# Kernel optimization log

Measured on AMD Instinct MI355X. Metric: run time of the kernel, lower is better.

Reference implementation:

```python
import jax, jax.numpy as jnp
import numpy as np

NEG_INF = -1e9  # Keras uses a large negative for masked logits


def setup_inputs() -> dict:
    key = jax.random.key(0)
    k1, k2, k3, k4, k5 = jax.random.split(key, 5)
    B, Tq, Tv, D, U = 8, 128, 128, 512, 1024
    query = jax.random.normal(k1, (B, Tq, D), dtype=jnp.float32)
    value = jax.random.normal(k2, (B, Tv, D), dtype=jnp.float32)
    mask = jnp.ones((B, Tv), dtype=bool)
    # Dense(units, use_bias=False) kernels and AdditiveAttention scale vector
    W1 = jax.random.normal(k3, (D, U), dtype=jnp.float32) * (1.0 / np.sqrt(D))
    W2 = jax.random.normal(k4, (D, U), dtype=jnp.float32) * (1.0 / np.sqrt(D))
    scale = jax.random.normal(k5, (U,), dtype=jnp.float32) * (1.0 / np.sqrt(U))
    return {"query": query, "value": value, "mask": mask,
            "W1": W1, "W2": W2, "scale": scale}


def reference(query, value, mask, W1, W2, scale):
    # Projections (Dense, no bias)
    wq = jnp.einsum('btd,du->btu', query, W1)   # [B, Tq, U]
    wk = jnp.einsum('bsd,du->bsu', value, W2)   # [B, Tv, U]
    # Additive (Bahdanau) scores: sum_u scale_u * tanh(wq + wk)
    # Materializes [B, Tq, Tv, U] broadcast-add like Keras AdditiveAttention.
    scores = jnp.einsum('u,btsu->bts', scale,
                        jnp.tanh(wq[:, :, None, :] + wk[:, None, :, :]))
    # value mask over key axis (query_mask is all-ones in the source -> no-op)
    scores = jnp.where(mask[:, None, :], scores, NEG_INF)
    attn = jax.nn.softmax(scores, axis=-1)       # [B, Tq, Tv]
    context = jnp.einsum('bts,bsd->btd', attn, value)  # [B, Tq, D]
    return context, attn
```

## Files before the change

kernel.cpp:

```cpp
#include <hip/hip_runtime.h>

#define B_  8
#define TQ  128
#define TV  128
#define DIM 512
#define UU  1024
#define NSPLIT 16
#define NP  (B_ * TQ * TV)
#define C2  2.885390081777927f

typedef __attribute__((ext_vector_type(8))) short     short8;
typedef __attribute__((ext_vector_type(4))) float     f32x4;
typedef __attribute__((ext_vector_type(4))) unsigned short us4;

__device__ __forceinline__ unsigned short bf16_rtne(float x) {
    unsigned u = __float_as_uint(x);
    unsigned r = u + 0x7FFF + ((u >> 16) & 1);
    return (unsigned short)(r >> 16);
}

__global__ __launch_bounds__(256) void k_prep(
    const float* __restrict__ Q, const float* __restrict__ Vv,
    const float* __restrict__ W1, const float* __restrict__ W2,
    unsigned short* __restrict__ Ab, unsigned short* __restrict__ Wh)
{
    __shared__ float ts[32][36];
    const int bx = blockIdx.x;
    const int t  = threadIdx.x;

    if (bx < 1024) {
        int idx = bx * 256 + t;
        int mat = idx >> 17;
        const float* src = mat ? Vv : Q;
        int off = (idx & 131071) * 4;
        float4 v = *(const float4*)&src[off];
        us4 h;
        h.x = bf16_rtne(v.x);
        h.y = bf16_rtne(v.y);
        h.z = bf16_rtne(v.z);
        h.w = bf16_rtne(v.w);
        *(us4*)&Ab[mat * 524288 + off] = h;
    } else {
        int b2   = bx - 1024;
        int mat  = b2 >> 9;
        int tile = b2 & 511;
        int n0 = (tile & 31) * 32;
        int k0 = (tile >> 5) * 32;
        const float* W = mat ? W2 : W1;

        int kk = t >> 3, n4 = (t & 7) * 4;
        float4 w = *(const float4*)&W[(k0 + kk) * UU + n0 + n4];
        ts[n4 + 0][kk] = w.x; ts[n4 + 1][kk] = w.y;
        ts[n4 + 2][kk] = w.z; ts[n4 + 3][kk] = w.w;
        __syncthreads();

        int nn = t >> 3, k4 = (t & 7) * 4;
        float4 v = *(const float4*)&ts[nn][k4];
        us4 h;
        h.x = bf16_rtne(v.x);
        h.y = bf16_rtne(v.y);
        h.z = bf16_rtne(v.z);
        h.w = bf16_rtne(v.w);
        unsigned off = mat * 524288 + (n0 + nn) * 512 + k0 + k4;
        *(us4*)&Wh[off] = h;
    }
}

#define PKP 72
__global__ __launch_bounds__(256) void k_proj(
    const unsigned short* __restrict__ Ab, const unsigned short* __restrict__ Bh,
    float* __restrict__ Eq, float* __restrict__ Ek)
{
    __shared__ short sAb[64 * PKP], sBh[64 * PKP];

    const int tid  = threadIdx.x;
    const int wave = tid >> 6;
    const int lane = tid & 63;

    const int flat = blockIdx.x;
    const int x    = flat & 7;
    const int j    = flat >> 3;
    const int pair = x * 4 + (j >> 4);
    const int nt   = pair & 15;
    const int mat  = pair >> 4;
    const int mt   = j & 15;
    const int m0   = mt * 64;
    const int n0   = nt * 64;

    const unsigned mb = mat * 524288u;
    const int wm = (wave & 1) * 32;
    const int wn = (wave >> 1) * 32;

    const int sm = tid >> 2, sg = tid & 3;
    const unsigned short* gA = Ab + mb + (m0 + sm) * 512;
    const unsigned short* gB = Bh + mb + (n0 + sm) * 512;
    const int so0 = sm * PKP + sg * 8;
    const int so1 = sm * PKP + 32 + sg * 8;

    const int fr = lane & 15, fq = lane >> 4;
    const int aOff0 = (wm + fr) * PKP + fq * 8;
    const int aOff1 = (wm + 16 + fr) * PKP + fq * 8;
    const int bOff0 = (wn + fr) * PKP + fq * 8;
    const int bOff1 = (wn + 16 + fr) * PKP + fq * 8;

    f32x4 acc00 = {0.f, 0.f, 0.f, 0.f};
    f32x4 acc01 = {0.f, 0.f, 0.f, 0.f};
    f32x4 acc10 = {0.f, 0.f, 0.f, 0.f};
    f32x4 acc11 = {0.f, 0.f, 0.f, 0.f};

    int4 rA0, rA1, rB0, rB1;
    #define LOADALL(K)                                                       \
        rA0 = *(const int4*)(gA + (K) + sg * 8);                             \
        rA1 = *(const int4*)(gA + (K) + 32 + sg * 8);                        \
        rB0 = *(const int4*)(gB + (K) + sg * 8);                             \
        rB1 = *(const int4*)(gB + (K) + 32 + sg * 8);

    LOADALL(0)

    #pragma unroll 1
    for (int kc = 0; kc < 8; ++kc) {
        *(int4*)&sAb[so0] = rA0;  *(int4*)&sAb[so1] = rA1;
        *(int4*)&sBh[so0] = rB0;  *(int4*)&sBh[so1] = rB1;
        __syncthreads();

        if (kc < 7) { LOADALL((kc + 1) * 64) }

        #pragma unroll
        for (int ks = 0; ks < 2; ++ks) {
            const int o = ks * 32;
            short8 a0 = *(const short8*)&sAb[aOff0 + o];
            short8 a1 = *(const short8*)&sAb[aOff1 + o];
            short8 b0 = *(const short8*)&sBh[bOff0 + o];
            short8 b1 = *(const short8*)&sBh[bOff1 + o];

            acc00 = __builtin_amdgcn_mfma_f32_16x16x32_bf16(a0, b0, acc00, 0, 0, 0);
            acc01 = __builtin_amdgcn_mfma_f32_16x16x32_bf16(a0, b1, acc01, 0, 0, 0);
            acc10 = __builtin_amdgcn_mfma_f32_16x16x32_bf16(a1, b0, acc10, 0, 0, 0);
            acc11 = __builtin_amdgcn_mfma_f32_16x16x32_bf16(a1, b1, acc11, 0, 0, 0);
        }
        __syncthreads();
    }
    #undef LOADALL

    float* C = mat ? Ek : Eq;
    #pragma unroll
    for (int r = 0; r < 4; ++r) {
        int row0 = m0 + wm + fq * 4 + r;
        int row1 = row0 + 16;
        int col0 = n0 + wn + fr;
        C[row0 * UU + col0]      = __builtin_amdgcn_exp2f(C2 * acc00[r]);
        C[row0 * UU + col0 + 16] = __builtin_amdgcn_exp2f(C2 * acc01[r]);
        C[row1 * UU + col0]      = __builtin_amdgcn_exp2f(C2 * acc10[r]);
        C[row1 * UU + col0 + 16] = __builtin_amdgcn_exp2f(C2 * acc11[r]);
    }
}
#undef PKP

__global__ __launch_bounds__(512, 4) void k_scores(
    const float* __restrict__ Eq, const float* __restrict__ Ek,
    const float* __restrict__ scale, float* __restrict__ part)
{
    __shared__ float qs[64][68];
    __shared__ float ks[64][68];
    __shared__ float ss[64];

    const int tid = threadIdx.x;
    const int tx  = tid & 15;
    const int ty  = tid >> 4;
    const int b   = blockIdx.z & 7;
    const int us  = blockIdx.z >> 3;
    const int t0  = blockIdx.y * 64;
    const int s0  = blockIdx.x * 64;
    const int u0  = us * (UU / NSPLIT);

    {
        const int r  = tid >> 3;
        const int c0 = (tid & 7) * 8;
        const float* srq = &Eq[(b * TQ + t0 + r) * UU + u0 + c0];
        const float* srk = &Ek[(b * TV + s0 + r) * UU + u0 + c0];
        const int rp = (r >> 2) | ((r & 3) << 4);
        *(float4*)&qs[r][c0]      = *(const float4*)(srq);
        *(float4*)&qs[r][c0 + 4]  = *(const float4*)(srq + 4);
        *(float4*)&ks[rp][c0]     = *(const float4*)(srk);
        *(float4*)&ks[rp][c0 + 4] = *(const float4*)(srk + 4);
        if (tid < 16)
            *(float4*)&ss[tid * 4] = *(const float4*)&scale[u0 + tid * 4];
    }
    __syncthreads();

    float acc[2][4] = {};

    #pragma unroll 2
    for (int u4 = 0; u4 < 16; ++u4) {
        float4 q[2], k[4];
        q[0] = *(const float4*)&qs[ty * 2][u4 * 4];
        q[1] = *(const float4*)&qs[ty * 2 + 1][u4 * 4];
        #pragma unroll
        for (int jj = 0; jj < 4; ++jj)
            k[jj] = *(const float4*)&ks[tx + (jj << 4)][u4 * 4];
        float4 sv = *(const float4*)&ss[u4 * 4];

        #pragma unroll
        for (int i = 0; i < 2; ++i) {
            #pragma unroll
            for (int jj = 0; jj < 4; ++jj) {
                float b1 = fmaf(q[i].x, k[jj].x, 1.f);
                float b2 = fmaf(q[i].y, k[jj].y, 1.f);
                float n1 = fmaf(sv.y, b1, sv.x * b2);
                acc[i][jj] = fmaf(n1, __builtin_amdgcn_rcpf(b1 * b2), acc[i][jj]);
                float b3 = fmaf(q[i].z, k[jj].z, 1.f);
                float b4 = fmaf(q[i].w, k[jj].w, 1.f);
                float n2 = fmaf(sv.w, b3, sv.z * b4);
                acc[i][jj] = fmaf(n2, __builtin_amdgcn_rcpf(b3 * b4), acc[i][jj]);
            }
        }
    }

    #pragma unroll
    for (int i = 0; i < 2; ++i) {
        float4 o = {acc[i][0], acc[i][1], acc[i][2], acc[i][3]};
        *(float4*)&part[us * NP + (b * TQ + t0 + ty * 2 + i) * TV + s0 + tx * 4] = o;
    }
}

__global__ __launch_bounds__(512) void k_ctx(
    const float* __restrict__ part, const int* __restrict__ mask,
    const float* __restrict__ Vv,
    float* __restrict__ attn, float* __restrict__ ctx)
{
    __shared__ float at[128][20];

    const int tid = threadIdx.x;
    const int dc  = blockIdx.x;
    const int tt  = blockIdx.y;
    const int b   = blockIdx.z;
    const int t0  = tt * 16;

    const int rg = tid >> 5;
    const int ln = tid & 31;
    const int base = (b * TQ + t0 + rg) * TV;

    float4 p4 = {0.f, 0.f, 0.f, 0.f};
    #pragma unroll
    for (int i = 0; i < NSPLIT; ++i) {
        float4 v = *(const float4*)&part[i * NP + base + ln * 4];
        p4.x += v.x; p4.y += v.y; p4.z += v.z; p4.w += v.w;
    }
    const int4 mk = *(const int4*)&mask[b * TV + ln * 4];
    float x[4];
    x[0] = mk.x ? -2.f * p4.x : -1e9f;
    x[1] = mk.y ? -2.f * p4.y : -1e9f;
    x[2] = mk.z ? -2.f * p4.z : -1e9f;
    x[3] = mk.w ? -2.f * p4.w : -1e9f;

    float m = fmaxf(fmaxf(x[0], x[1]), fmaxf(x[2], x[3]));
    #pragma unroll
    for (int o = 16; o > 0; o >>= 1) m = fmaxf(m, __shfl_xor(m, o, 32));
    const float L2E = 1.4426950408889634f;
    float e[4], sum = 0.f;
    #pragma unroll
    for (int j = 0; j < 4; ++j) {
        e[j] = __builtin_amdgcn_exp2f((x[j] - m) * L2E);
        sum += e[j];
    }
    #pragma unroll
    for (int o = 16; o > 0; o >>= 1) sum += __shfl_xor(sum, o, 32);
    const float r = __builtin_amdgcn_rcpf(sum);

    float4 av = {e[0] * r, e[1] * r, e[2] * r, e[3] * r};
    at[ln * 4 + 0][rg] = av.x;
    at[ln * 4 + 1][rg] = av.y;
    at[ln * 4 + 2][rg] = av.z;
    at[ln * 4 + 3][rg] = av.w;
    if (dc == 0) *(float4*)&attn[base + ln * 4] = av;
    __syncthreads();

    const int d  = (tid & 127) + dc * 128;
    const int tg = tid >> 7;
    float acc[4] = {};
    const float* vp = &Vv[b * TV * DIM + d];
    #pragma unroll 4
    for (int s = 0; s < TV; ++s) {
        float v  = vp[s * DIM];
        float4 a = *(const float4*)&at[s][tg * 4];
        acc[0] = fmaf(a.x, v, acc[0]);
        acc[1] = fmaf(a.y, v, acc[1]);
        acc[2] = fmaf(a.z, v, acc[2]);
        acc[3] = fmaf(a.w, v, acc[3]);
    }
    #pragma unroll
    for (int j = 0; j < 4; ++j) {
        int t = t0 + tg * 4 + j;
        ctx[(b * TQ + t) * DIM + d] = acc[j];
    }
}

extern "C" void kernel_launch(void* const* d_in, const int* in_sizes, int n_in,
                              void* d_out, int out_size, void* d_ws, size_t ws_size,
                              hipStream_t stream)
{
    const float* query = (const float*)d_in[0];
    const float* value = (const float*)d_in[1];
    const int*   mask  = (const int*)d_in[2];
    const float* W1    = (const float*)d_in[3];
    const float* W2    = (const float*)d_in[4];
    const float* scale = (const float*)d_in[5];

    float* out  = (float*)d_out;
    float* ctx  = out;
    float* attn = out + B_ * TQ * DIM;

    float* Eq   = (float*)d_ws;
    float* Ek   = Eq + 1024 * 1024;
    float* part = Ek + 1024 * 1024;
    unsigned short* Ab = (unsigned short*)(part + NSPLIT * NP);
    unsigned short* Wh = Ab + 2 * 1024 * 512;

    hipLaunchKernelGGL(k_prep,   dim3(2048),             dim3(256), 0, stream,
                       query, value, W1, W2, Ab, Wh);
    hipLaunchKernelGGL(k_proj,   dim3(512),              dim3(256), 0, stream,
                       Ab, Wh, Eq, Ek);
    hipLaunchKernelGGL(k_scores, dim3(2, 2, 8 * NSPLIT), dim3(512), 0, stream,
                       Eq, Ek, scale, part);
    hipLaunchKernelGGL(k_ctx,    dim3(4, 8, 8),          dim3(512), 0, stream,
                       part, mask, value, attn, ctx);
}
```

Before: 110.3 us.

## Use packed FP32 FMA in scores kernel with transposed K tile and 4x4 outputs

Rewrites the scores kernel to use packed 2-wide FP32 FMA (v_pk_fma_f32 on CDNA) over pairs of key columns, with K stored transposed in shared memory so adjacent keys are contiguous. Each thread now computes 4x4 outputs instead of 2x4, and the block shrinks from 512 to 256 threads. This aims to cut VALU instruction count and LDS loads per output. The cost is more registers per thread, fewer threads per block, and a transposed scalar LDS store pattern that may cause bank conflicts.

```diff
diff --git a/kernel.cpp b/kernel.cpp
--- a/kernel.cpp
+++ b/kernel.cpp
@@ -11,12 +11,17 @@
 
 typedef __attribute__((ext_vector_type(8))) short     short8;
 typedef __attribute__((ext_vector_type(4))) float     f32x4;
+typedef __attribute__((ext_vector_type(2))) float     f32x2;
 typedef __attribute__((ext_vector_type(4))) unsigned short us4;
 
 __device__ __forceinline__ unsigned short bf16_rtne(float x) {
     unsigned u = __float_as_uint(x);
     unsigned r = u + 0x7FFF + ((u >> 16) & 1);
     return (unsigned short)(r >> 16);
+}
+
+__device__ __forceinline__ f32x2 pkfma(f32x2 a, f32x2 b, f32x2 c) {
+    return __builtin_elementwise_fma(a, b, c);
 }
 
 __global__ __launch_bounds__(256) void k_prep(
@@ -156,12 +161,12 @@
 }
 #undef PKP
 
-__global__ __launch_bounds__(512, 4) void k_scores(
+__global__ __launch_bounds__(256) void k_scores(
     const float* __restrict__ Eq, const float* __restrict__ Ek,
     const float* __restrict__ scale, float* __restrict__ part)
 {
     __shared__ float qs[64][68];
-    __shared__ float ks[64][68];
+    __shared__ float ksT[64][68];
     __shared__ float ss[64];
 
     const int tid = threadIdx.x;
@@ -174,52 +179,70 @@
     const int u0  = us * (UU / NSPLIT);
 
     {
-        const int r  = tid >> 3;
-        const int c0 = (tid & 7) * 8;
+        const int r  = tid >> 2;
+        const int c0 = (tid & 3) * 16;
         const float* srq = &Eq[(b * TQ + t0 + r) * UU + u0 + c0];
         const float* srk = &Ek[(b * TV + s0 + r) * UU + u0 + c0];
-        const int rp = (r >> 2) | ((r & 3) << 4);
-        *(float4*)&qs[r][c0]      = *(const float4*)(srq);
-        *(float4*)&qs[r][c0 + 4]  = *(const float4*)(srq + 4);
-        *(float4*)&ks[rp][c0]     = *(const float4*)(srk);
-        *(float4*)&ks[rp][c0 + 4] = *(const float4*)(srk + 4);
+        #pragma unroll
+        for (int i = 0; i < 4; ++i) {
+            *(float4*)&qs[r][c0 + i * 4] = *(const float4*)(srq + i * 4);
+            float4 kv = *(const float4*)(srk + i * 4);
+            ksT[c0 + i * 4 + 0][r] = kv.x;
+            ksT[c0 + i * 4 + 1][r] = kv.y;
+            ksT[c0 + i * 4 + 2][r] = kv.z;
+            ksT[c0 + i * 4 + 3][r] = kv.w;
+        }
         if (tid < 16)
             *(float4*)&ss[tid * 4] = *(const float4*)&scale[u0 + tid * 4];
     }
     __syncthreads();
 
-    float acc[2][4] = {};
+    f32x2 acc[4][2] = {};
+    const f32x2 one2 = {1.f, 1.f};
 
     #pragma unroll 2
     for (int u4 = 0; u4 < 16; ++u4) {
-        float4 q[2], k[4];
-        q[0] = *(const float4*)&qs[ty * 2][u4 * 4];
-        q[1] = *(const float4*)&qs[ty * 2 + 1][u4 * 4];
+        f32x2 kA[4][2];
         #pragma unroll
-        for (int jj = 0; jj < 4; ++jj)
-            k[jj] = *(const float4*)&ks[tx + (jj << 4)][u4 * 4];
-        float4 sv = *(const float4*)&ss[u4 * 4];
+        for (int uu = 0; uu < 4; ++uu) {
+            float4 kv = *(const float4*)&ksT[u4 * 4 + uu][tx * 4];
+            kA[uu][0] = (f32x2){kv.x, kv.y};
+            kA[uu][1] = (f32x2){kv.z, kv.w};
+        }
+        const float4 sv = *(const float4*)&ss[u4 * 4];
+        const f32x2 sL0 = {sv.x, sv.x}, sH0 = {sv.y, sv.y};
+        const f32x2 sL1 = {sv.z, sv.z}, sH1 = {sv.w, sv.w};
 
         #pragma unroll
-        for (int i = 0; i < 2; ++i) {
+        for (int i = 0; i < 4; ++i) {
+            const float4 qv = *(const float4*)&qs[ty * 4 + i][u4 * 4];
+            const f32x2 qL0 = {qv.x, qv.x}, qH0 = {qv.y, qv.y};
+            const f32x2 qL1 = {qv.z, qv.z}, qH1 = {qv.w, qv.w};
+
             #pragma unroll
-            for (int jj = 0; jj < 4; ++jj) {
-                float b1 = fmaf(q[i].x, k[jj].x, 1.f);
-                float b2 = fmaf(q[i].y, k[jj].y, 1.f);
-                float n1 = fmaf(sv.y, b1, sv.x * b2);
-                acc[i][jj] = fmaf(n1, __builtin_amdgcn_rcpf(b1 * b2), acc[i][jj]);
-                float b3 = fmaf(q[i].z, k[jj].z, 1.f);
-                float b4 = fmaf(q[i].w, k[jj].w, 1.f);
-                float n2 = fmaf(sv.w, b3, sv.z * b4);
-                acc[i][jj] = fmaf(n2, __builtin_amdgcn_rcpf(b3 * b4), acc[i][jj]);
+            for (int jp = 0; jp < 2; ++jp) {
+                f32x2 b1 = pkfma(qL0, kA[0][jp], one2);
+                f32x2 b2 = pkfma(qH0, kA[1][jp], one2);
+                f32x2 p  = b1 * b2;
+                f32x2 n  = pkfma(sH0, b1, sL0 * b2);
+                f32x2 r  = {__builtin_amdgcn_rcpf(p.x),
+                            __builtin_amdgcn_rcpf(p.y)};
+                acc[i][jp] = pkfma(n, r, acc[i][jp]);
+                f32x2 b3 = pkfma(qL1, kA[2][jp], one2);
+                f32x2 b4 = pkfma(qH1, kA[3][jp], one2);
+                f32x2 p2 = b3 * b4;
+                f32x2 n2 = pkfma(sH1, b3, sL1 * b4);
+                f32x2 r2 = {__builtin_amdgcn_rcpf(p2.x),
+                            __builtin_amdgcn_rcpf(p2.y)};
+                acc[i][jp] = pkfma(n2, r2, acc[i][jp]);
             }
         }
     }
 
     #pragma unroll
-    for (int i = 0; i < 2; ++i) {
-        float4 o = {acc[i][0], acc[i][1], acc[i][2], acc[i][3]};
-        *(float4*)&part[us * NP + (b * TQ + t0 + ty * 2 + i) * TV + s0 + tx * 4] = o;
+    for (int i = 0; i < 4; ++i) {
+        float4 o = {acc[i][0].x, acc[i][0].y, acc[i][1].x, acc[i][1].y};
+        *(float4*)&part[us * NP + (b * TQ + t0 + ty * 4 + i) * TV + s0 + tx * 4] = o;
     }
 }
 
@@ -320,7 +343,7 @@
                        query, value, W1, W2, Ab, Wh);
     hipLaunchKernelGGL(k_proj,   dim3(512),              dim3(256), 0, stream,
                        Ab, Wh, Eq, Ek);
-    hipLaunchKernelGGL(k_scores, dim3(2, 2, 8 * NSPLIT), dim3(512), 0, stream,
+    hipLaunchKernelGGL(k_scores, dim3(2, 2, 8 * NSPLIT), dim3(256), 0, stream,
                        Eq, Ek, scale, part);
     hipLaunchKernelGGL(k_ctx,    dim3(4, 8, 8),          dim3(512), 0, stream,
                        part, mask, value, attn, ctx);
```

Result: no change. 110.7 us (+0.4%).
